# Performance work log

Hardware: AMD Instinct MI355X
Metric: run time of the kernel (lower is better)

Reference implementation:

```python
import jax, jax.numpy as jnp
import numpy as np

N_NODES = 20000
N_EDGES = 320000
NF = 128   # num_node_feats
EF = 32    # num_edge_feats
CF = 3     # num_coord_feats
H = 512    # hidden_dim


def setup_inputs() -> dict:
    key = jax.random.key(0)
    ks = jax.random.split(key, 20)
    s = lambda k, shape, fan_in: jax.random.normal(k, shape, jnp.float32) / np.sqrt(fan_in)
    return {
        "hfeats": jax.random.normal(ks[0], (N_NODES, NF), jnp.float32),
        "cfeats": jax.random.normal(ks[1], (N_NODES, CF), jnp.float32),
        "efeats": jax.random.normal(ks[2], (N_EDGES, EF), jnp.float32),
        "src": jax.random.randint(ks[3], (N_EDGES,), 0, N_NODES, jnp.int32),
        "dst": jax.random.randint(ks[4], (N_EDGES,), 0, N_NODES, jnp.int32),
        # node_expansion: Linear(NF, H)
        "Wn": s(ks[5], (NF, H), NF), "bn": jnp.zeros((H,), jnp.float32),
        # edge_expansion: Linear(EF, H)
        "We": s(ks[6], (EF, H), EF), "be": jnp.zeros((H,), jnp.float32),
        # coord_expansion: Linear(CF, H)
        "Wc": s(ks[7], (CF, H), CF), "bc": jnp.zeros((H,), jnp.float32),
        # combination_reduction_nfeats: Linear(H,H) -> CELU -> Linear(H,NF) -> CELU
        "Wn1": s(ks[8], (H, H), H), "bn1": jnp.zeros((H,), jnp.float32),
        "Wn2": s(ks[9], (H, NF), H), "bn2": jnp.zeros((NF,), jnp.float32),
        # combination_reduction_efeats: Linear(H, EF) -> CELU
        "Weo": s(ks[10], (H, EF), H), "beo": jnp.zeros((EF,), jnp.float32),
        # combination_reduction_cfeats: Linear(H, CF) -> CELU
        "Wco": s(ks[11], (H, CF), H), "bco": jnp.zeros((CF,), jnp.float32),
    }


def reference(hfeats, cfeats, efeats, src, dst,
              Wn, bn, We, be, Wc, bc,
              Wn1, bn1, Wn2, bn2, Weo, beo, Wco, bco):
    celu = jax.nn.celu
    n_nodes = hfeats.shape[0]
    # Feature expansions (Linear + CELU)
    h = celu(hfeats @ Wn + bn)   # [N, H]
    e = celu(efeats @ We + be)   # [E, H]
    c = celu(cfeats @ Wc + bc)   # [N, H]
    # edge_udf: x = |c_dst - c_src| * (h_src * e)   -> [E, H]
    x = jnp.abs(c[dst] - c[src]) * (h[src] * e)
    # update_all(copy_e, sum): scatter-sum edge messages to dst nodes
    k = jax.ops.segment_sum(x, dst, num_segments=n_nodes)  # [N, H]
    # Residual combination-reductions
    h_out = hfeats + celu(celu(k @ Wn1 + bn1) @ Wn2 + bn2)
    e_out = efeats + celu(e @ Weo + beo)
    c_out = cfeats + celu(c @ Wco + bco)
    return (h_out, c_out, e_out)
```

## Files before the change

kernel.cpp:

```cpp
#include <hip/hip_runtime.h>
#include <hip/hip_bf16.h>

#define NF 128
#define EF 32
#define CF 3
#define H  512
#define EB 32

typedef __attribute__((ext_vector_type(8))) short bf16x8;
typedef __attribute__((ext_vector_type(4))) float f32x4;

__device__ __forceinline__ float celu_f(float x) {
    return fmaxf(x, __expf(fminf(x, 0.0f)) - 1.0f);
}
__device__ __forceinline__ uint cvtpk(float lo, float hi) {
    uint r;
    asm("v_cvt_pk_bf16_f32 %0, %1, %2" : "=v"(r) : "v"(lo), "v"(hi));
    return r;
}
__device__ __forceinline__ bf16x8 pack8(float4 v0, float4 v1) {
    union { uint4 u; bf16x8 b; } r;
    r.u.x = cvtpk(v0.x, v0.y); r.u.y = cvtpk(v0.z, v0.w);
    r.u.z = cvtpk(v1.x, v1.y); r.u.w = cvtpk(v1.z, v1.w);
    return r.b;
}
__device__ __forceinline__ float b2f(ushort s) {
    union { uint u; float f; } v; v.u = ((uint)s) << 16; return v.f;
}
__device__ __forceinline__ void unpack4(uint2 v, float* o) {
    union { uint u; float f; } x;
    x.u = v.x << 16;          o[0] = x.f;
    x.u = v.x & 0xffff0000u;  o[1] = x.f;
    x.u = v.y << 16;          o[2] = x.f;
    x.u = v.y & 0xffff0000u;  o[3] = x.f;
}

__global__ void setup_kernel(const float* __restrict__ We, const float* __restrict__ Weo,
                             const float* __restrict__ Wn, const float* __restrict__ Wn1,
                             const float* __restrict__ Wn2, const int* __restrict__ dst,
                             ushort* __restrict__ Wet, ushort* __restrict__ Weot,
                             ushort* __restrict__ Wnt, ushort* __restrict__ Wn1t,
                             ushort* __restrict__ Wn2t, int* __restrict__ cnt,
                             int n_edges) {
    int i = blockIdx.x * 256 + threadIdx.x;
    if (i < H * EF) {
        int j = i / EF, k = i % EF;
        Wet[i] = (ushort)cvtpk(We[(size_t)k * H + j], 0.f);
        int o = i / H, j2 = i % H;
        Weot[i] = (ushort)cvtpk(Weo[(size_t)j2 * EF + o], 0.f);
    }
    if (i < H * NF) {
        int o = i >> 7, k = i & 127;
        Wnt[i] = (ushort)cvtpk(Wn[(size_t)k * H + o], 0.f);
        int o2 = i >> 9, k2 = i & 511;
        Wn2t[i] = (ushort)cvtpk(Wn2[(size_t)k2 * NF + o2], 0.f);
    }
    if (i < H * H) {
        int o = i >> 9, k = i & 511;
        Wn1t[i] = (ushort)cvtpk(Wn1[(size_t)k * H + o], 0.f);
    }
    const int nthreads = gridDim.x * 256;
    for (int e = i; e < n_edges; e += nthreads)
        atomicAdd(&cnt[dst[e]], 1);
}

__global__ void scan_kernel(int* __restrict__ cnt, int n_nodes) {
    __shared__ int part[1024];
    const int t = threadIdx.x;
    const int per = (n_nodes + 1023) / 1024;
    int s = 0;
    for (int i = 0; i < per; ++i) {
        int idx = t * per + i;
        if (idx < n_nodes) s += cnt[idx];
    }
    part[t] = s;
    __syncthreads();
    for (int off = 1; off < 1024; off <<= 1) {
        int v = (t >= off) ? part[t - off] : 0;
        __syncthreads();
        part[t] += v;
        __syncthreads();
    }
    int acc = part[t] - s;
    for (int i = 0; i < per; ++i) {
        int idx = t * per + i;
        if (idx < n_nodes) {
            int c = cnt[idx];
            cnt[idx] = acc;
            acc += c;
        }
    }
}

__global__ __launch_bounds__(256) void node_expand_kernel(
        const float* __restrict__ hfeats, const float* __restrict__ cfeats,
        const ushort* __restrict__ Wnt, const float* __restrict__ bn,
        const float* __restrict__ Wc, const float* __restrict__ bc,
        ushort* __restrict__ hc, int n_nodes,
        const int* __restrict__ dst, int* __restrict__ cursor,
        int* __restrict__ perm, int n_edges, int nNE) {
    const int t = threadIdx.x;
    if (blockIdx.x >= nNE) {
        int i = (blockIdx.x - nNE) * 256 + t;
        if (i < n_edges) {
            int pos = atomicAdd(&cursor[dst[i]], 1);
            perm[pos] = i;
        }
        return;
    }
    __shared__ ushort hf[32 * NF];
    __shared__ float cf[32][4];
    const int lane = t & 63;
    const int w = t >> 6;
    const int node0 = blockIdx.x * 32;

    for (int i = t; i < 32 * 16; i += 256) {
        int row = i >> 4, g = i & 15;
        int node = node0 + row; if (node >= n_nodes) node = n_nodes - 1;
        const float* p = hfeats + (size_t)node * NF + g * 8;
        float4 v0 = *(const float4*)p;
        float4 v1 = *(const float4*)(p + 4);
        ((bf16x8*)hf)[row * 16 + (g ^ (row & 7))] = pack8(v0, v1);
    }
    for (int i = t; i < 32 * CF; i += 256) {
        int n = i / CF, k = i % CF;
        int node = node0 + n; if (node >= n_nodes) node = n_nodes - 1;
        cf[n][k] = cfeats[(size_t)node * CF + k];
    }
    __syncthreads();

    const int ar = lane & 15;
    const int hi = lane >> 4;
    const int ak = hi * 8;

    f32x4 acc[2][8];
    #pragma unroll
    for (int nt = 0; nt < 2; ++nt)
        #pragma unroll
        for (int q = 0; q < 8; ++q) { f32x4 z = {0.f,0.f,0.f,0.f}; acc[nt][q] = z; }

    for (int kstep = 0; kstep < NF / 32; ++kstep) {
        bf16x8 nfrag[2];
        #pragma unroll
        for (int nt = 0; nt < 2; ++nt) {
            int r = nt * 16 + ar;
            int g = kstep * 4 + hi;
            nfrag[nt] = ((const bf16x8*)hf)[r * 16 + (g ^ (r & 7))];
        }
        #pragma unroll
        for (int q = 0; q < 8; ++q) {
            bf16x8 wf = *(const bf16x8*)(Wnt + (size_t)((w * 8 + q) * 16 + ar) * NF + kstep * 32 + ak);
            acc[0][q] = __builtin_amdgcn_mfma_f32_16x16x32_bf16(wf, nfrag[0], acc[0][q], 0, 0, 0);
            acc[1][q] = __builtin_amdgcn_mfma_f32_16x16x32_bf16(wf, nfrag[1], acc[1][q], 0, 0, 0);
        }
    }
    #pragma unroll
    for (int q = 0; q < 8; ++q) {
        const int jbase = (w * 8 + q) * 16 + hi * 4;
        const float4 bv = *(const float4*)(bn + jbase);
        #pragma unroll
        for (int nt = 0; nt < 2; ++nt) {
            int node = node0 + nt * 16 + ar;
            if (node < n_nodes) {
                uint2 pk;
                pk.x = cvtpk(celu_f(acc[nt][q][0] + bv.x), celu_f(acc[nt][q][1] + bv.y));
                pk.y = cvtpk(celu_f(acc[nt][q][2] + bv.z), celu_f(acc[nt][q][3] + bv.w));
                *(uint2*)(hc + (size_t)node * 1024 + (jbase >> 2) * 8) = pk;
            }
        }
    }

    for (int i = t; i < 32 * 64; i += 256) {
        int n = i >> 6, gj = i & 63;
        int node = node0 + n;
        if (node < n_nodes) {
            int j = gj * 8;
            float c0 = cf[n][0], c1 = cf[n][1], c2 = cf[n][2];
            float v[8];
            #pragma unroll
            for (int u = 0; u < 8; ++u)
                v[u] = celu_f(bc[j + u] + c0 * Wc[j + u] + c1 * Wc[H + j + u] + c2 * Wc[2 * H + j + u]);
            uint2 p0, p1;
            p0.x = cvtpk(v[0], v[1]); p0.y = cvtpk(v[2], v[3]);
            p1.x = cvtpk(v[4], v[5]); p1.y = cvtpk(v[6], v[7]);
            *(uint2*)(hc + (size_t)node * 1024 + (2 * gj) * 8 + 4) = p0;
            *(uint2*)(hc + (size_t)node * 1024 + (2 * gj + 1) * 8 + 4) = p1;
        }
    }
}

__global__ __launch_bounds__(512, 4) void edge_kernel(
        const float* __restrict__ efeats,
        const int* __restrict__ src, const int* __restrict__ dst,
        const int* __restrict__ perm,
        const ushort* __restrict__ Wet, const float* __restrict__ be,
        const ushort* __restrict__ Weot, const float* __restrict__ beo,
        const ushort* __restrict__ hc,
        float* __restrict__ k_acc, float* __restrict__ e_out, int n_edges,
        int nEB,
        const float* __restrict__ cfeats, const float* __restrict__ Wco,
        const float* __restrict__ bco, float* __restrict__ c_out, int n_nodes) {
    const int t = threadIdx.x;
    const int lane = t & 63;
    const int w = t >> 6;

    if (blockIdx.x >= nEB) {
        const int node = (blockIdx.x - nEB) * 8 + w;
        if (node >= n_nodes) return;
        uint2 cv0 = *(const uint2*)(hc + (size_t)node * 1024 + (2 * lane) * 8 + 4);
        uint2 cv1 = *(const uint2*)(hc + (size_t)node * 1024 + (2 * lane + 1) * 8 + 4);
        float cv[8];
        unpack4(cv0, cv);
        unpack4(cv1, cv + 4);
        float a0 = 0.f, a1 = 0.f, a2 = 0.f;
        #pragma unroll
        for (int u = 0; u < 8; ++u) {
            int j = lane * 8 + u;
            a0 += cv[u] * Wco[j * CF + 0];
            a1 += cv[u] * Wco[j * CF + 1];
            a2 += cv[u] * Wco[j * CF + 2];
        }
        #pragma unroll
        for (int m = 32; m >= 1; m >>= 1) {
            a0 += __shfl_xor(a0, m);
            a1 += __shfl_xor(a1, m);
            a2 += __shfl_xor(a2, m);
        }
        if (lane < 3) {
            float s = (lane == 0) ? a0 : (lane == 1) ? a1 : a2;
            c_out[(size_t)node * CF + lane] = cfeats[(size_t)node * CF + lane] + celu_f(bco[lane] + s);
        }
        return;
    }

    __shared__ ushort e512[EB * 512];
    __shared__ int s_perm[EB], s_src[EB], s_dst[EB];

    const int q = nEB >> 3, r = nEB & 7;
    const int xcd = blockIdx.x & 7, sub = blockIdx.x >> 3;
    const int bid = (xcd < r ? xcd * (q + 1) : r * (q + 1) + (xcd - r) * q) + sub;
    const int e0 = bid * EB;

    if (t < EB) {
        int e = e0 + t;
        int pe = (e < n_edges) ? perm[e] : -1;
        s_perm[t] = pe;
        s_src[t] = (pe >= 0) ? src[pe] : 0;
        s_dst[t] = (pe >= 0) ? dst[pe] : -1;
    }
    __syncthreads();

    const int ar = lane & 15;
    const int hi = lane >> 4;
    const int ak = hi * 8;

    const int grp = t >> 7;
    const int ct = t & 127;
    const int j0 = ct * 4;
    const int g = j0 >> 3, go = j0 & 7;
    const int ebase = grp * 16;
    uint4 svb[2][4];
    uint2 cdb[2][4];
    uint2 evb[2][4];
    if (w < 4) {
        #pragma unroll
        for (int j = 0; j < 4; ++j) {
            const int e = ebase + j;
            const int s_ = s_src[e];
            int dc = s_dst[e]; dc = (dc < 0) ? 0 : dc;
            svb[0][j] = *(const uint4*)(hc + (size_t)s_ * 1024 + ct * 8);
            cdb[0][j] = *(const uint2*)(hc + (size_t)dc * 1024 + ct * 8 + 4);
        }
    }

    {
        bf16x8 wfrag[4];
        #pragma unroll
        for (int qq = 0; qq < 4; ++qq)
            wfrag[qq] = *(const bf16x8*)(Wet + (size_t)((w * 4 + qq) * 16 + ar) * EF + ak);
        #pragma unroll
        for (int et = 0; et < 2; ++et) {
            bf16x8 efrag;
            {
                int pe = s_perm[et * 16 + ar];
                if (pe < 0) pe = 0;
                const float* p = efeats + (size_t)pe * EF + ak;
                float4 v0 = *(const float4*)p;
                float4 v1 = *(const float4*)(p + 4);
                efrag = pack8(v0, v1);
            }
            f32x4 acc[4];
            #pragma unroll
            for (int qq = 0; qq < 4; ++qq) { f32x4 z = {0.f,0.f,0.f,0.f}; acc[qq] = z; }
            #pragma unroll
            for (int qq = 0; qq < 4; ++qq)
                acc[qq] = __builtin_amdgcn_mfma_f32_16x16x32_bf16(wfrag[qq], efrag, acc[qq], 0, 0, 0);
            const int e_l = et * 16 + ar;
            #pragma unroll
            for (int qq = 0; qq < 4; ++qq) {
                const int jbase = (w * 4 + qq) * 16 + hi * 4;
                const float4 bv = *(const float4*)(be + jbase);
                uint2 pk;
                pk.x = cvtpk(celu_f(acc[qq][0] + bv.x), celu_f(acc[qq][1] + bv.y));
                pk.y = cvtpk(celu_f(acc[qq][2] + bv.z), celu_f(acc[qq][3] + bv.w));
                const int gs = (jbase >> 3) ^ (e_l & 7);
                *(uint2*)(&e512[e_l * 512 + gs * 8 + (jbase & 7)]) = pk;
            }
        }
    }
    __syncthreads();

    if (w < 4) {
        float a_[4];
        a_[0] = a_[1] = a_[2] = a_[3] = 0.f;
        int cur = -1;

        #pragma unroll
        for (int j = 0; j < 4; ++j) {
            const int e = ebase + j;
            evb[0][j] = *(const uint2*)(&e512[e * 512 + (g ^ (e & 7)) * 8 + go]);
        }

        #pragma unroll
        for (int c = 0; c < 4; ++c) {
            const int cb = c & 1, nb = cb ^ 1;
            if (c < 3) {
                #pragma unroll
                for (int j = 0; j < 4; ++j) {
                    const int e = ebase + (c + 1) * 4 + j;
                    const int s_ = s_src[e];
                    int dc = s_dst[e]; dc = (dc < 0) ? 0 : dc;
                    svb[nb][j] = *(const uint4*)(hc + (size_t)s_ * 1024 + ct * 8);
                    cdb[nb][j] = *(const uint2*)(hc + (size_t)dc * 1024 + ct * 8 + 4);
                    evb[nb][j] = *(const uint2*)(&e512[e * 512 + (g ^ (e & 7)) * 8 + go]);
                }
            }
            #pragma unroll
            for (int j = 0; j < 4; ++j) {
                const int e = ebase + c * 4 + j;
                const int d = __builtin_amdgcn_readfirstlane(s_dst[e]);
                if (d != cur) {
                    if (cur >= 0) {
                        #pragma unroll
                        for (int u = 0; u < 4; ++u)
                            atomicAdd(&k_acc[(size_t)cur * H + j0 + u], a_[u]);
                        a_[0] = a_[1] = a_[2] = a_[3] = 0.f;
                    }
                    cur = d;
                }
                if (d >= 0) {
                    float hs_[4], cs_[4], cd_[4], ev_[4];
                    uint2 hv; hv.x = svb[cb][j].x; hv.y = svb[cb][j].y;
                    uint2 cv; cv.x = svb[cb][j].z; cv.y = svb[cb][j].w;
                    unpack4(hv, hs_);
                    unpack4(cv, cs_);
                    unpack4(cdb[cb][j], cd_);
                    unpack4(evb[cb][j], ev_);
                    #pragma unroll
                    for (int u = 0; u < 4; ++u)
                        a_[u] += fabsf(cd_[u] - cs_[u]) * (hs_[u] * ev_[u]);
                }
            }
        }
        if (cur >= 0) {
            #pragma unroll
            for (int u = 0; u < 4; ++u)
                atomicAdd(&k_acc[(size_t)cur * H + j0 + u], a_[u]);
        }
    } else {
        const int wc = w - 4;
        const int ot = wc & 1, et = wc >> 1;
        const int e_l = et * 16 + ar;
        f32x4 accc = {0.f, 0.f, 0.f, 0.f};
        #pragma unroll
        for (int kt = 0; kt < 16; ++kt) {
            bf16x8 wfC = *(const bf16x8*)(Weot + (size_t)(ot * 16 + ar) * H + kt * 32 + ak);
            const int gs = (kt * 4 + hi) ^ (e_l & 7);
            bf16x8 b = *(const bf16x8*)(&e512[e_l * 512 + gs * 8]);
            accc = __builtin_amdgcn_mfma_f32_16x16x32_bf16(wfC, b, accc, 0, 0, 0);
        }
        const int pe = s_perm[e_l];
        if (pe >= 0) {
            const int obase = ot * 16 + hi * 4;
            const float4 bo = *(const float4*)(beo + obase);
            size_t idx = (size_t)pe * EF + obase;
            float4 ef4 = *(const float4*)(efeats + idx);
            float4 o;
            o.x = ef4.x + celu_f(accc[0] + bo.x);
            o.y = ef4.y + celu_f(accc[1] + bo.y);
            o.z = ef4.z + celu_f(accc[2] + bo.z);
            o.w = ef4.w + celu_f(accc[3] + bo.w);
            *(float4*)(e_out + idx) = o;
        }
    }
}

__global__ __launch_bounds__(256) void node_out_kernel(
        const float* __restrict__ hfeats, const float* __restrict__ k_acc,
        const ushort* __restrict__ Wn1t, const float* __restrict__ bn1,
        const ushort* __restrict__ Wn2t, const float* __restrict__ bn2,
        float* __restrict__ h_out, int n_nodes) {
    __shared__ ushort kt_s[32 * H];
    const int t = threadIdx.x;
    const int lane = t & 63;
    const int w = t >> 6;
    const int node0 = blockIdx.x * 32;

    for (int i = t; i < 32 * 64; i += 256) {
        int row = i >> 6, g = i & 63;
        int node = node0 + row; if (node >= n_nodes) node = n_nodes - 1;
        const float* p = k_acc + (size_t)node * H + g * 8;
        float4 v0 = *(const float4*)p;
        float4 v1 = *(const float4*)(p + 4);
        ((bf16x8*)kt_s)[row * 64 + (g ^ (row & 7))] = pack8(v0, v1);
    }
    __syncthreads();

    const int ar = lane & 15;
    const int hi = lane >> 4;
    const int ak = hi * 8;

    f32x4 acc[2][8];
    #pragma unroll
    for (int nt = 0; nt < 2; ++nt)
        #pragma unroll
        for (int q = 0; q < 8; ++q) { f32x4 z = {0.f,0.f,0.f,0.f}; acc[nt][q] = z; }

    for (int kstep = 0; kstep < H / 32; ++kstep) {
        bf16x8 kfrag[2];
        #pragma unroll
        for (int nt = 0; nt < 2; ++nt) {
            int rr = nt * 16 + ar;
            int g = kstep * 4 + hi;
            kfrag[nt] = ((const bf16x8*)kt_s)[rr * 64 + (g ^ (rr & 7))];
        }
        #pragma unroll
        for (int q = 0; q < 8; ++q) {
            bf16x8 wf = *(const bf16x8*)(Wn1t + (size_t)((w * 8 + q) * 16 + ar) * H + kstep * 32 + ak);
            acc[0][q] = __builtin_amdgcn_mfma_f32_16x16x32_bf16(wf, kfrag[0], acc[0][q], 0, 0, 0);
            acc[1][q] = __builtin_amdgcn_mfma_f32_16x16x32_bf16(wf, kfrag[1], acc[1][q], 0, 0, 0);
        }
    }
    __syncthreads();

    #pragma unroll
    for (int q = 0; q < 8; ++q) {
        const int jbase = (w * 8 + q) * 16 + hi * 4;
        const float4 bv = *(const float4*)(bn1 + jbase);
        #pragma unroll
        for (int nt = 0; nt < 2; ++nt) {
            const int rr = nt * 16 + ar;
            uint2 pk;
            pk.x = cvtpk(celu_f(acc[nt][q][0] + bv.x), celu_f(acc[nt][q][1] + bv.y));
            pk.y = cvtpk(celu_f(acc[nt][q][2] + bv.z), celu_f(acc[nt][q][3] + bv.w));
            const int gs = (jbase >> 3) ^ (rr & 7);
            *(uint2*)(&kt_s[rr * 512 + gs * 8 + (jbase & 7)]) = pk;
        }
    }
    __syncthreads();

    f32x4 acc2[2][2];
    #pragma unroll
    for (int nt = 0; nt < 2; ++nt)
        #pragma unroll
        for (int ct = 0; ct < 2; ++ct) { f32x4 z = {0.f,0.f,0.f,0.f}; acc2[nt][ct] = z; }

    for (int kstep = 0; kstep < H / 32; ++kstep) {
        bf16x8 tfrag[2];
        #pragma unroll
        for (int nt = 0; nt < 2; ++nt) {
            int rr = nt * 16 + ar;
            int g = kstep * 4 + hi;
            tfrag[nt] = ((const bf16x8*)kt_s)[rr * 64 + (g ^ (rr & 7))];
        }
        #pragma unroll
        for (int ct = 0; ct < 2; ++ct) {
            bf16x8 wf = *(const bf16x8*)(Wn2t + (size_t)((w * 2 + ct) * 16 + ar) * H + kstep * 32 + ak);
            acc2[0][ct] = __builtin_amdgcn_mfma_f32_16x16x32_bf16(wf, tfrag[0], acc2[0][ct], 0, 0, 0);
            acc2[1][ct] = __builtin_amdgcn_mfma_f32_16x16x32_bf16(wf, tfrag[1], acc2[1][ct], 0, 0, 0);
        }
    }
    #pragma unroll
    for (int ct = 0; ct < 2; ++ct) {
        const int jbase = (w * 2 + ct) * 16 + hi * 4;
        const float4 bv = *(const float4*)(bn2 + jbase);
        #pragma unroll
        for (int nt = 0; nt < 2; ++nt) {
            const int node = node0 + nt * 16 + ar;
            if (node < n_nodes) {
                size_t idx = (size_t)node * NF + jbase;
                float4 hf4 = *(const float4*)(hfeats + idx);
                float4 o;
                o.x = hf4.x + celu_f(acc2[nt][ct][0] + bv.x);
                o.y = hf4.y + celu_f(acc2[nt][ct][1] + bv.y);
                o.z = hf4.z + celu_f(acc2[nt][ct][2] + bv.z);
                o.w = hf4.w + celu_f(acc2[nt][ct][3] + bv.w);
                *(float4*)(h_out + idx) = o;
            }
        }
    }
}

extern "C" void kernel_launch(void* const* d_in, const int* in_sizes, int n_in,
                              void* d_out, int out_size, void* d_ws, size_t ws_size,
                              hipStream_t stream) {
    const float* hfeats = (const float*)d_in[0];
    const float* cfeats = (const float*)d_in[1];
    const float* efeats = (const float*)d_in[2];
    const int*   src    = (const int*)d_in[3];
    const int*   dst    = (const int*)d_in[4];
    const float* Wn  = (const float*)d_in[5];  const float* bn  = (const float*)d_in[6];
    const float* We  = (const float*)d_in[7];  const float* be  = (const float*)d_in[8];
    const float* Wc  = (const float*)d_in[9];  const float* bc  = (const float*)d_in[10];
    const float* Wn1 = (const float*)d_in[11]; const float* bn1 = (const float*)d_in[12];
    const float* Wn2 = (const float*)d_in[13]; const float* bn2 = (const float*)d_in[14];
    const float* Weo = (const float*)d_in[15]; const float* beo = (const float*)d_in[16];
    const float* Wco = (const float*)d_in[17]; const float* bco = (const float*)d_in[18];

    const int n_nodes = in_sizes[0] / NF;
    const int n_edges = in_sizes[2] / EF;

    float*  k_buf = (float*)d_ws;
    ushort* hc    = (ushort*)(k_buf + (size_t)n_nodes * H);
    ushort* Wet   = hc + (size_t)n_nodes * H * 2;
    ushort* Weot  = Wet + (size_t)H * EF;
    ushort* Wnt   = Weot + (size_t)H * EF;
    ushort* Wn1t  = Wnt + (size_t)H * NF;
    ushort* Wn2t  = Wn1t + (size_t)H * H;
    int*    cnt   = (int*)(Wn2t + (size_t)NF * H);
    int*    perm  = cnt + n_nodes;

    float* h_out = (float*)d_out;
    float* c_out = h_out + (size_t)n_nodes * NF;
    float* e_out = c_out + (size_t)n_nodes * CF;

    hipMemsetAsync(k_buf, 0, (size_t)n_nodes * H * sizeof(float), stream);
    hipMemsetAsync(cnt, 0, (size_t)n_nodes * sizeof(int), stream);

    setup_kernel<<<(H * H + 255) / 256, 256, 0, stream>>>(
        We, Weo, Wn, Wn1, Wn2, dst, Wet, Weot, Wnt, Wn1t, Wn2t, cnt, n_edges);

    scan_kernel<<<1, 1024, 0, stream>>>(cnt, n_nodes);

    const int nNE = (n_nodes + 31) / 32;
    const int nSC = (n_edges + 255) / 256;
    node_expand_kernel<<<nNE + nSC, 256, 0, stream>>>(
        hfeats, cfeats, Wnt, bn, Wc, bc, hc, n_nodes,
        dst, cnt, perm, n_edges, nNE);

    const int nEB = (n_edges + EB - 1) / EB;
    const int nCO = (n_nodes + 7) / 8;
    edge_kernel<<<nEB + nCO, 512, 0, stream>>>(
        efeats, src, dst, perm, Wet, be, Weot, beo, hc, k_buf, e_out, n_edges,
        nEB, cfeats, Wco, bco, c_out, n_nodes);

    node_out_kernel<<<(n_nodes + 31) / 32, 256, 0, stream>>>(
        hfeats, k_buf, Wn1t, bn1, Wn2t, bn2, h_out, n_nodes);
}
```

Before: 439.6 us.

## Fuse k_buf zeroing into setup kernel and enlarge node_out tile to 64 nodes

The memset of the k accumulation buffer is removed, and setup_kernel now zeroes it with a grid-stride float4 loop, saving a separate memset launch. node_out_kernel is retiled to 64 nodes per block with 512 threads. Each weight fragment loaded from global memory is now reused across four node tiles instead of two, which halves the Wn1/Wn2 global weight traffic per node. The cost is double the LDS per block (64 KB), which limits occupancy, plus higher register pressure under the launch_bounds hint.

```diff
diff --git a/kernel.cpp b/kernel.cpp
--- a/kernel.cpp
+++ b/kernel.cpp
@@ -41,7 +41,7 @@
                              ushort* __restrict__ Wet, ushort* __restrict__ Weot,
                              ushort* __restrict__ Wnt, ushort* __restrict__ Wn1t,
                              ushort* __restrict__ Wn2t, int* __restrict__ cnt,
-                             int n_edges) {
+                             float* __restrict__ k_buf, int n_edges, int nk4) {
     int i = blockIdx.x * 256 + threadIdx.x;
     if (i < H * EF) {
         int j = i / EF, k = i % EF;
@@ -60,6 +60,9 @@
         Wn1t[i] = (ushort)cvtpk(Wn1[(size_t)k * H + o], 0.f);
     }
     const int nthreads = gridDim.x * 256;
+    float4 z4 = {0.f, 0.f, 0.f, 0.f};
+    for (int p = i; p < nk4; p += nthreads)
+        ((float4*)k_buf)[p] = z4;
     for (int e = i; e < n_edges; e += nthreads)
         atomicAdd(&cnt[dst[e]], 1);
 }
@@ -395,18 +398,18 @@
     }
 }
 
-__global__ __launch_bounds__(256) void node_out_kernel(
+__global__ __launch_bounds__(512, 4) void node_out_kernel(
         const float* __restrict__ hfeats, const float* __restrict__ k_acc,
         const ushort* __restrict__ Wn1t, const float* __restrict__ bn1,
         const ushort* __restrict__ Wn2t, const float* __restrict__ bn2,
         float* __restrict__ h_out, int n_nodes) {
-    __shared__ ushort kt_s[32 * H];
+    __shared__ ushort kt_s[64 * H];
     const int t = threadIdx.x;
     const int lane = t & 63;
     const int w = t >> 6;
-    const int node0 = blockIdx.x * 32;
-
-    for (int i = t; i < 32 * 64; i += 256) {
+    const int node0 = blockIdx.x * 64;
+
+    for (int i = t; i < 64 * 64; i += 512) {
         int row = i >> 6, g = i & 63;
         int node = node0 + row; if (node >= n_nodes) node = n_nodes - 1;
         const float* p = k_acc + (size_t)node * H + g * 8;
@@ -420,35 +423,36 @@
     const int hi = lane >> 4;
     const int ak = hi * 8;
 
-    f32x4 acc[2][8];
+    f32x4 acc[4][4];
     #pragma unroll
-    for (int nt = 0; nt < 2; ++nt)
-        #pragma unroll
-        for (int q = 0; q < 8; ++q) { f32x4 z = {0.f,0.f,0.f,0.f}; acc[nt][q] = z; }
+    for (int nt = 0; nt < 4; ++nt)
+        #pragma unroll
+        for (int q = 0; q < 4; ++q) { f32x4 z = {0.f,0.f,0.f,0.f}; acc[nt][q] = z; }
 
     for (int kstep = 0; kstep < H / 32; ++kstep) {
-        bf16x8 kfrag[2];
-        #pragma unroll
-        for (int nt = 0; nt < 2; ++nt) {
+        bf16x8 kfrag[4];
+        #pragma unroll
+        for (int nt = 0; nt < 4; ++nt) {
             int rr = nt * 16 + ar;
             int g = kstep * 4 + hi;
             kfrag[nt] = ((const bf16x8*)kt_s)[rr * 64 + (g ^ (rr & 7))];
         }
         #pragma unroll
-        for (int q = 0; q < 8; ++q) {
-            bf16x8 wf = *(const bf16x8*)(Wn1t + (size_t)((w * 8 + q) * 16 + ar) * H + kstep * 32 + ak);
-            acc[0][q] = __builtin_amdgcn_mfma_f32_16x16x32_bf16(wf, kfrag[0], acc[0][q], 0, 0, 0);
-            acc[1][q] = __builtin_amdgcn_mfma_f32_16x16x32_bf16(wf, kfrag[1], acc[1][q], 0, 0, 0);
+        for (int q = 0; q < 4; ++q) {
+            bf16x8 wf = *(const bf16x8*)(Wn1t + (size_t)((w * 4 + q) * 16 + ar) * H + kstep * 32 + ak);
+            #pragma unroll
+            for (int nt = 0; nt < 4; ++nt)
+                acc[nt][q] = __builtin_amdgcn_mfma_f32_16x16x32_bf16(wf, kfrag[nt], acc[nt][q], 0, 0, 0);
         }
     }
     __syncthreads();
 
     #pragma unroll
-    for (int q = 0; q < 8; ++q) {
-        const int jbase = (w * 8 + q) * 16 + hi * 4;
+    for (int q = 0; q < 4; ++q) {
+        const int jbase = (w * 4 + q) * 16 + hi * 4;
         const float4 bv = *(const float4*)(bn1 + jbase);
         #pragma unroll
-        for (int nt = 0; nt < 2; ++nt) {
+        for (int nt = 0; nt < 4; ++nt) {
             const int rr = nt * 16 + ar;
             uint2 pk;
             pk.x = cvtpk(celu_f(acc[nt][q][0] + bv.x), celu_f(acc[nt][q][1] + bv.y));
@@ -459,42 +463,34 @@
     }
     __syncthreads();
 
-    f32x4 acc2[2][2];
+    f32x4 acc2[4];
     #pragma unroll
-    for (int nt = 0; nt < 2; ++nt)
-        #pragma unroll
-        for (int ct = 0; ct < 2; ++ct) { f32x4 z = {0.f,0.f,0.f,0.f}; acc2[nt][ct] = z; }
+    for (int nt = 0; nt < 4; ++nt) { f32x4 z = {0.f,0.f,0.f,0.f}; acc2[nt] = z; }
 
     for (int kstep = 0; kstep < H / 32; ++kstep) {
-        bf16x8 tfrag[2];
-        #pragma unroll
-        for (int nt = 0; nt < 2; ++nt) {
+        bf16x8 wf = *(const bf16x8*)(Wn2t + (size_t)(w * 16 + ar) * H + kstep * 32 + ak);
+        #pragma unroll
+        for (int nt = 0; nt < 4; ++nt) {
             int rr = nt * 16 + ar;
             int g = kstep * 4 + hi;
-            tfrag[nt] = ((const bf16x8*)kt_s)[rr * 64 + (g ^ (rr & 7))];
-        }
-        #pragma unroll
-        for (int ct = 0; ct < 2; ++ct) {
-            bf16x8 wf = *(const bf16x8*)(Wn2t + (size_t)((w * 2 + ct) * 16 + ar) * H + kstep * 32 + ak);
-            acc2[0][ct] = __builtin_amdgcn_mfma_f32_16x16x32_bf16(wf, tfrag[0], acc2[0][ct], 0, 0, 0);
-            acc2[1][ct] = __builtin_amdgcn_mfma_f32_16x16x32_bf16(wf, tfrag[1], acc2[1][ct], 0, 0, 0);
-        }
-    }
-    #pragma unroll
-    for (int ct = 0; ct < 2; ++ct) {
-        const int jbase = (w * 2 + ct) * 16 + hi * 4;
+            bf16x8 tfrag = ((const bf16x8*)kt_s)[rr * 64 + (g ^ (rr & 7))];
+            acc2[nt] = __builtin_amdgcn_mfma_f32_16x16x32_bf16(wf, tfrag, acc2[nt], 0, 0, 0);
+        }
+    }
+    {
+        const int jbase = w * 16 + hi * 4;
         const float4 bv = *(const float4*)(bn2 + jbase);
         #pragma unroll
-        for (int nt = 0; nt < 2; ++nt) {
+        for (int nt = 0; nt < 4; ++nt) {
             const int node = node0 + nt * 16 + ar;
             if (node < n_nodes) {
                 size_t idx = (size_t)node * NF + jbase;
                 float4 hf4 = *(const float4*)(hfeats + idx);
                 float4 o;
-                o.x = hf4.x + celu_f(acc2[nt][ct][0] + bv.x);
-                o.y = hf4.y + celu_f(acc2[nt][ct][1] + bv.y);
-                o.z = hf4.z + celu_f(acc2[nt][ct][2] + bv.z);
-                o.w = hf4.w + celu_f(acc2[nt][ct][3] + bv.w);
+                o.x = hf4.x + celu_f(acc2[nt][0] + bv.x);
+                o.y = hf4.y + celu_f(acc2[nt][1] + bv.y);
+                o.z = hf4.z + celu_f(acc2[nt][2] + bv.z);
+                o.w = hf4.w + celu_f(acc2[nt][3] + bv.w);
                 *(float4*)(h_out + idx) = o;
             }
         }
@@ -534,11 +530,12 @@
     float* c_out = h_out + (size_t)n_nodes * NF;
     float* e_out = c_out + (size_t)n_nodes * CF;
 
-    hipMemsetAsync(k_buf, 0, (size_t)n_nodes * H * sizeof(float), stream);
     hipMemsetAsync(cnt, 0, (size_t)n_nodes * sizeof(int), stream);
 
+    const int nk4 = (n_nodes * H) / 4;
     setup_kernel<<<(H * H + 255) / 256, 256, 0, stream>>>(
-        We, Weo, Wn, Wn1, Wn2, dst, Wet, Weot, Wnt, Wn1t, Wn2t, cnt, n_edges);
+        We, Weo, Wn, Wn1, Wn2, dst, Wet, Weot, Wnt, Wn1t, Wn2t, cnt, k_buf,
+        n_edges, nk4);
 
     scan_kernel<<<1, 1024, 0, stream>>>(cnt, n_nodes);
 
@@ -554,6 +551,6 @@
         efeats, src, dst, perm, Wet, be, Weot, beo, hc, k_buf, e_out, n_edges,
         nEB, cfeats, Wco, bco, c_out, n_nodes);
 
-    node_out_kernel<<<(n_nodes + 31) / 32, 256, 0, stream>>>(
+    node_out_kernel<<<(n_nodes + 63) / 64, 512, 0, stream>>>(
         hfeats, k_buf, Wn1t, bn1, Wn2t, bn2, h_out, n_nodes);
 }
```

New measurement: 420.1 us. -4.5%, faster.
